# Kernel tuning notes

Hardware: AMD Instinct MI355X
Metric: run time of the kernel (lower is better)

## Reference

```python
import jax, jax.numpy as jnp
import numpy as np

N, C, H, W = 8, 128, 64, 64
S, K = 2, 5  # scale_factor, k_up
NK = (S * K) ** 2  # 100 predicted kernel channels
BN_EPS = 1e-5


def _conv(x, w, b, pad):
    y = jax.lax.conv_general_dilated(
        x, w, window_strides=(1, 1), padding=[(pad, pad), (pad, pad)],
        dimension_numbers=('NCHW', 'OIHW', 'NCHW'))
    return y + b[None, :, None, None]


def setup_inputs() -> dict:
    key = jax.random.key(0)
    ks = jax.random.split(key, 12)
    rn = lambda k, s, sc=0.05: jax.random.normal(k, s, jnp.float32) * sc
    return {
        'x': jax.random.normal(ks[0], (N, C, H, W), jnp.float32),
        'w_enc': rn(ks[1], (64, C, 3, 3)), 'b_enc': rn(ks[2], (64,)),
        'bn_gamma': jnp.ones((64,), jnp.float32), 'bn_beta': jnp.zeros((64,), jnp.float32),
        'bn_mean': rn(ks[3], (64,)), 'bn_var': jnp.abs(rn(ks[4], (64,))) + 1.0,
        'w_kp': rn(ks[5], (NK, 64, 1, 1)), 'b_kp': rn(ks[6], (NK,)),
        'w_g1': rn(ks[7], (64, 64, 3, 3)), 'b_g1': rn(ks[8], (64,)),
        'w_g2': rn(ks[9], (NK, 64, 1, 1)), 'b_g2': rn(ks[10], (NK,)),
    }


def reference(x, w_enc, b_enc, bn_gamma, bn_beta, bn_mean, bn_var,
              w_kp, b_kp, w_g1, b_g1, w_g2, b_g2):
    # content encoder: conv3x3 -> BN (inference stats) -> ReLU
    c = _conv(x, w_enc, b_enc, 1)
    inv = jax.lax.rsqrt(bn_var + BN_EPS)
    content = jax.nn.relu((c - bn_mean[None, :, None, None]) * (bn_gamma * inv)[None, :, None, None]
                          + bn_beta[None, :, None, None])
    # kernel and gate predictors
    kernel = _conv(content, w_kp, b_kp, 0)                     # (N, 100, H, W)
    gate = jax.nn.sigmoid(_conv(jax.nn.relu(_conv(content, w_g1, b_g1, 1)), w_g2, b_g2, 0))
    ker = jax.nn.softmax(kernel * gate, axis=1)                # softmax over all 100 chans
    ker = ker.reshape(N, K, K, S, S, H, W)
    # replicate-pad and gather KxK neighborhoods (channel-major, row-major kernel order = F.unfold)
    p = K // 2
    x_pad = jnp.pad(x, ((0, 0), (0, 0), (p, p), (p, p)), mode='edge')
    patches = jnp.stack([x_pad[:, :, i:i + H, j:j + W]
                         for i in range(K) for j in range(K)], axis=2)  # (N, C, K*K, H, W)
    patches = patches.reshape(N, C, K, K, H, W)
    # content-aware reassembly; target layout (N, C, H, S, W, S) for pixel-shuffle reshape
    out = jnp.einsum('ncijhw,nijsthw->nchswt', patches, ker)
    return out.reshape(N, C, H * S, W * S)
```

## Files before the change

### kernel.cpp

```cpp
#include <hip/hip_runtime.h>
#include <hip/hip_bf16.h>


typedef __attribute__((ext_vector_type(8))) short short8;
typedef __attribute__((ext_vector_type(4))) float f32x4;

__global__ __launch_bounds__(256) void x_to_bf_nhwc(const float* __restrict__ x,
                                                    __hip_bfloat16* __restrict__ xb) {
    __shared__ float ls[128 * 65];
    const int blk = blockIdx.x, n = blk >> 6, h = blk & 63;
    const int tid = threadIdx.x;
    for (int idx = tid; idx < 8192; idx += 256) {
        int ci = idx >> 6, w = idx & 63;
        ls[ci * 65 + w] = x[((n * 128 + ci) * 64 + h) * 64 + w];
    }
    __syncthreads();
    for (int idx = tid; idx < 8192; idx += 256) {
        int w = idx >> 7, ci = idx & 127;
        xb[((n * 64 + h) * 64 + w) * 128 + ci] = __float2bfloat16(ls[ci * 65 + w]);
    }
}

__global__ void w_to_bf(const float* __restrict__ w, __hip_bfloat16* __restrict__ o,
                        int CI, int total) {
    int idx = blockIdx.x * 256 + threadIdx.x;
    if (idx >= total) return;
    int ci = idx % CI;
    int t = idx / CI;
    int co = t & 63;
    int p = t >> 6;
    o[idx] = __float2bfloat16(w[(co * CI + ci) * 9 + p]);
}

template<int CIN>
__global__ __launch_bounds__(256) void conv3x3_mfma(
    const __hip_bfloat16* __restrict__ xb, const __hip_bfloat16* __restrict__ wt,
    const float* __restrict__ bias, const float* __restrict__ gamma,
    const float* __restrict__ beta, const float* __restrict__ mean,
    const float* __restrict__ var,
    float* __restrict__ out_f32,
    __hip_bfloat16* __restrict__ out_bf)
{
    constexpr int CINP = CIN + 8;
    __shared__ short xs[3 * 66 * CINP];
    const int blk = blockIdx.x, n = blk >> 6, h = blk & 63;
    const int tid = threadIdx.x;
    const int lane = tid & 63, wave = tid >> 6;
    const int m = lane & 15, q = lane >> 4;
    const int co0 = wave * 16;

    const short8 zero8 = {0, 0, 0, 0, 0, 0, 0, 0};
    for (int idx = tid; idx < 3 * 66 * (CIN / 8); idx += 256) {
        int c8 = idx % (CIN / 8);
        int p = idx / (CIN / 8);
        int r = p / 66, w = p % 66;
        int hh = h + r - 1, wc = w - 1;
        short8 v = zero8;
        if ((unsigned)hh < 64u && (unsigned)wc < 64u)
            v = *(const short8*)&xb[(((n * 64 + hh) * 64 + wc) * CIN) + c8 * 8];
        *(short8*)&xs[(r * 66 + w) * CINP + c8 * 8] = v;
    }
    __syncthreads();

    f32x4 acc[4] = {{0.f, 0.f, 0.f, 0.f}, {0.f, 0.f, 0.f, 0.f},
                    {0.f, 0.f, 0.f, 0.f}, {0.f, 0.f, 0.f, 0.f}};
    const int kbase = q * 8;
    #pragma unroll
    for (int kh = 0; kh < 3; ++kh) {
        #pragma unroll
        for (int kw = 0; kw < 3; ++kw) {
            const __hip_bfloat16* wp = &wt[((kh * 3 + kw) * 64 + co0 + m) * CIN + kbase];
            const short* xp = &xs[(kh * 66 + kw + m) * CINP + kbase];
            #pragma unroll
            for (int kc = 0; kc < CIN / 32; ++kc) {
                short8 bfrag = *(const short8*)&wp[kc * 32];
                #pragma unroll
                for (int mt = 0; mt < 4; ++mt) {
                    short8 afrag = *(const short8*)&xp[mt * 16 * CINP + kc * 32];
                    acc[mt] = __builtin_amdgcn_mfma_f32_16x16x32_bf16(
                        afrag, bfrag, acc[mt], 0, 0, 0);
                }
            }
        }
    }

    const int c = co0 + m;
    float sc, sh;
    if (gamma) {
        float inv = rsqrtf(var[c] + 1e-5f);
        sc = gamma[c] * inv;
        sh = (bias[c] - mean[c]) * sc + beta[c];
    } else {
        sc = 1.f;
        sh = bias[c];
    }
    #pragma unroll
    for (int mt = 0; mt < 4; ++mt) {
        const int w0 = mt * 16 + q * 4;
        float ov[4];
        #pragma unroll
        for (int r = 0; r < 4; ++r)
            ov[r] = fmaxf(fmaf(acc[mt][r], sc, sh), 0.f);
        if (out_f32) {
            #pragma unroll
            for (int r = 0; r < 4; ++r)
                out_f32[((n * 64 + h) * 64 + (w0 + r)) * 64 + c] = ov[r];
        }
        if (out_bf) {
            #pragma unroll
            for (int r = 0; r < 4; ++r)
                out_bf[((n * 64 + h) * 64 + (w0 + r)) * 64 + c] = __float2bfloat16(ov[r]);
        }
    }
}

__global__ __launch_bounds__(256) void predictor_k(
    const __hip_bfloat16* __restrict__ cb, const float* __restrict__ g1,
    const float* __restrict__ wkp, const float* __restrict__ bkp,
    const float* __restrict__ wg2, const float* __restrict__ bg2,
    float* __restrict__ ker)
{
    __shared__ float cs[64 * 68];
    __shared__ float gs[64 * 68];
    __shared__ float wsm[100 * 64];
    __shared__ float redm[256], reds[256];
    const int blk = blockIdx.x;
    const int n = blk >> 6, h = blk & 63;
    const int tid = threadIdx.x;
    const int w = tid & 63, qg = tid >> 6;

    for (int idx = tid; idx < 4096; idx += 256) {
        int ww = idx >> 6, ci = idx & 63;
        const int gidx = ((n * 64 + h) * 64 + ww) * 64 + ci;
        cs[ww * 68 + ci] = __bfloat162float(cb[gidx]);
        gs[ww * 68 + ci] = g1[gidx];
    }
    for (int idx = tid; idx < 6400; idx += 256) wsm[idx] = wkp[idx];
    __syncthreads();

    float ka[25], ga[25];
    #pragma unroll
    for (int j = 0; j < 25; ++j) ka[j] = bkp[qg * 25 + j];
    for (int ci = 0; ci < 64; ci += 4) {
        const float4 cv = *(const float4*)&cs[w * 68 + ci];
        #pragma unroll
        for (int j = 0; j < 25; ++j) {
            const float4 wv = *(const float4*)&wsm[(qg * 25 + j) * 64 + ci];
            ka[j] = fmaf(cv.x, wv.x, ka[j]);
            ka[j] = fmaf(cv.y, wv.y, ka[j]);
            ka[j] = fmaf(cv.z, wv.z, ka[j]);
            ka[j] = fmaf(cv.w, wv.w, ka[j]);
        }
    }
    __syncthreads();
    for (int idx = tid; idx < 6400; idx += 256) wsm[idx] = wg2[idx];
    __syncthreads();
    #pragma unroll
    for (int j = 0; j < 25; ++j) ga[j] = bg2[qg * 25 + j];
    for (int ci = 0; ci < 64; ci += 4) {
        const float4 gv = *(const float4*)&gs[w * 68 + ci];
        #pragma unroll
        for (int j = 0; j < 25; ++j) {
            const float4 wv = *(const float4*)&wsm[(qg * 25 + j) * 64 + ci];
            ga[j] = fmaf(gv.x, wv.x, ga[j]);
            ga[j] = fmaf(gv.y, wv.y, ga[j]);
            ga[j] = fmaf(gv.z, wv.z, ga[j]);
            ga[j] = fmaf(gv.w, wv.w, ga[j]);
        }
    }

    float p[25], m = -1e30f;
    #pragma unroll
    for (int j = 0; j < 25; ++j) {
        float s = 1.f / (1.f + __expf(-ga[j]));
        p[j] = ka[j] * s;
        m = fmaxf(m, p[j]);
    }
    redm[tid] = m;
    __syncthreads();
    m = fmaxf(fmaxf(redm[w], redm[64 + w]), fmaxf(redm[128 + w], redm[192 + w]));
    float ssum = 0.f;
    #pragma unroll
    for (int j = 0; j < 25; ++j) { p[j] = __expf(p[j] - m); ssum += p[j]; }
    reds[tid] = ssum;
    __syncthreads();
    ssum = reds[w] + reds[64 + w] + reds[128 + w] + reds[192 + w];
    const float r = 1.f / ssum;

    float* sm = cs;
    #pragma unroll
    for (int j = 0; j < 25; ++j) sm[w * 100 + qg * 25 + j] = p[j] * r;
    __syncthreads();
    const int base = (n * 64 + h) * 6400;
    for (int idx = tid; idx < 6400; idx += 256) ker[base + idx] = sm[idx];
}

__global__ __launch_bounds__(256) void reassembly_k(
    const float* __restrict__ x, const float* __restrict__ ker,
    float* __restrict__ out)
{
    constexpr int CT = 16;
    __shared__ float xls[CT][5][68];
    __shared__ float kls[64 * 108];
    const int blk = blockIdx.x;
    const int cb = blk & 7, h = (blk >> 3) & 63, n = blk >> 9;
    const int c0 = cb * CT;
    const int tid = threadIdx.x;
    const int w = tid & 63, cgq = tid >> 6;

    for (int idx = tid; idx < CT * 5 * 68; idx += 256) {
        int ci = idx / 340, r = idx % 340;
        int rr = r / 68, col = r % 68;
        int sr = min(max(h - 2 + rr, 0), 63);
        int sc = min(max(col - 2, 0), 63);
        xls[ci][rr][col] = x[((n * 128 + c0 + ci) * 64 + sr) * 64 + sc];
    }
    {
        const int base = (n * 64 + h) * 6400;
        for (int idx = tid; idx < 6400; idx += 256) {
            int ww = idx / 100, q = idx % 100;
            kls[ww * 108 + q] = ker[base + idx];
        }
    }
    __syncthreads();

    float acc[4][4] = {};
    #pragma unroll
    for (int i = 0; i < 5; ++i) {
        #pragma unroll
        for (int j = 0; j < 5; ++j) {
            const float4 kv = *(const float4*)&kls[w * 108 + (i * 5 + j) * 4];
            #pragma unroll
            for (int cc = 0; cc < 4; ++cc) {
                const float xv = xls[cgq * 4 + cc][i][w + j];
                acc[cc][0] = fmaf(xv, kv.x, acc[cc][0]);
                acc[cc][1] = fmaf(xv, kv.y, acc[cc][1]);
                acc[cc][2] = fmaf(xv, kv.z, acc[cc][2]);
                acc[cc][3] = fmaf(xv, kv.w, acc[cc][3]);
            }
        }
    }
    #pragma unroll
    for (int cc = 0; cc < 4; ++cc) {
        const int c = c0 + cgq * 4 + cc;
        #pragma unroll
        for (int s = 0; s < 2; ++s) {
            float2 v = make_float2(acc[cc][s * 2], acc[cc][s * 2 + 1]);
            *(float2*)&out[((n * 128 + c) * 128 + 2 * h + s) * 128 + 2 * w] = v;
        }
    }
}

extern "C" void kernel_launch(void* const* d_in, const int* in_sizes, int n_in,
                              void* d_out, int out_size, void* d_ws, size_t ws_size,
                              hipStream_t stream) {
    const float* x     = (const float*)d_in[0];
    const float* w_enc = (const float*)d_in[1];
    const float* b_enc = (const float*)d_in[2];
    const float* gamma = (const float*)d_in[3];
    const float* beta  = (const float*)d_in[4];
    const float* mean  = (const float*)d_in[5];
    const float* var   = (const float*)d_in[6];
    const float* w_kp  = (const float*)d_in[7];
    const float* b_kp  = (const float*)d_in[8];
    const float* w_g1  = (const float*)d_in[9];
    const float* b_g1  = (const float*)d_in[10];
    const float* w_g2  = (const float*)d_in[11];
    const float* b_g2  = (const float*)d_in[12];
    float* out = (float*)d_out;

    float* g1r = (float*)d_ws;
    float* ker = g1r + 2097152;
    __hip_bfloat16* xb  = (__hip_bfloat16*)(ker + 3276800);
    __hip_bfloat16* cbf = xb + 4194304;
    __hip_bfloat16* wtt = cbf + 2097152;
    __hip_bfloat16* wgt = wtt + 73728;

    x_to_bf_nhwc<<<512, 256, 0, stream>>>(x, xb);
    w_to_bf<<<288, 256, 0, stream>>>(w_enc, wtt, 128, 73728);
    w_to_bf<<<144, 256, 0, stream>>>(w_g1, wgt, 64, 36864);

    conv3x3_mfma<128><<<512, 256, 0, stream>>>(
        xb, wtt, b_enc, gamma, beta, mean, var, nullptr, cbf);
    conv3x3_mfma<64><<<512, 256, 0, stream>>>(
        cbf, wgt, b_g1, nullptr, nullptr, nullptr, nullptr, g1r, nullptr);

    predictor_k<<<512, 256, 0, stream>>>(cbf, g1r, w_kp, b_kp, w_g2, b_g2, ker);
    reassembly_k<<<4096, 256, 0, stream>>>(x, ker, out);
}
```

Baseline: 217.1 us.

## Split conv rows into half-width blocks and stream reassembly kernels from global

The 3x3 MFMA convs now process half a row per block, with waves tiled 2x2 over width and output channels, doubling the grid to 1024 blocks and shrinking shared memory. Reassembly loads x rows with float4 vector loads plus explicit edge replication, and reads the per-pixel kernel weights straight from global memory instead of staging them in LDS. This targets occupancy, shared-memory footprint and load efficiency, at the cost of more halo reloads in the conv and uncached strided global reads of ker in reassembly. The CINP padding also changes from 8 to 4, which affects LDS bank conflicts and short8 alignment.

```diff
diff --git a/kernel.cpp b/kernel.cpp
--- a/kernel.cpp
+++ b/kernel.cpp
@@ -41,75 +41,67 @@
     float* __restrict__ out_f32,
     __hip_bfloat16* __restrict__ out_bf)
 {
-    constexpr int CINP = CIN + 8;
-    __shared__ short xs[3 * 66 * CINP];
-    const int blk = blockIdx.x, n = blk >> 6, h = blk & 63;
+    constexpr int CINP = CIN + 4;
+    __shared__ short xs[3 * 34 * CINP];
+    const int blk = blockIdx.x;
+    const int wh = blk & 1, h = (blk >> 1) & 63, n = blk >> 7;
     const int tid = threadIdx.x;
     const int lane = tid & 63, wave = tid >> 6;
     const int m = lane & 15, q = lane >> 4;
-    const int co0 = wave * 16;
+    const int mt = wave >> 1;
+    const int nh = wave & 1;
 
     const short8 zero8 = {0, 0, 0, 0, 0, 0, 0, 0};
-    for (int idx = tid; idx < 3 * 66 * (CIN / 8); idx += 256) {
+    for (int idx = tid; idx < 3 * 34 * (CIN / 8); idx += 256) {
         int c8 = idx % (CIN / 8);
         int p = idx / (CIN / 8);
-        int r = p / 66, w = p % 66;
-        int hh = h + r - 1, wc = w - 1;
+        int r = p / 34, cx = p % 34;
+        int hh = h + r - 1, gc = wh * 32 - 1 + cx;
         short8 v = zero8;
-        if ((unsigned)hh < 64u && (unsigned)wc < 64u)
-            v = *(const short8*)&xb[(((n * 64 + hh) * 64 + wc) * CIN) + c8 * 8];
-        *(short8*)&xs[(r * 66 + w) * CINP + c8 * 8] = v;
-    }
-    __syncthreads();
-
-    f32x4 acc[4] = {{0.f, 0.f, 0.f, 0.f}, {0.f, 0.f, 0.f, 0.f},
-                    {0.f, 0.f, 0.f, 0.f}, {0.f, 0.f, 0.f, 0.f}};
+        if ((unsigned)hh < 64u && (unsigned)gc < 64u)
+            v = *(const short8*)&xb[(((n * 64 + hh) * 64 + gc) * CIN) + c8 * 8];
+        *(short8*)&xs[(r * 34 + cx) * CINP + c8 * 8] = v;
+    }
+    __syncthreads();
+
+    f32x4 acc[2] = {{0.f, 0.f, 0.f, 0.f}, {0.f, 0.f, 0.f, 0.f}};
     const int kbase = q * 8;
     #pragma unroll
     for (int kh = 0; kh < 3; ++kh) {
         #pragma unroll
         for (int kw = 0; kw < 3; ++kw) {
-            const __hip_bfloat16* wp = &wt[((kh * 3 + kw) * 64 + co0 + m) * CIN + kbase];
-            const short* xp = &xs[(kh * 66 + kw + m) * CINP + kbase];
+            const short* xp = &xs[(kh * 34 + mt * 16 + m + kw) * CINP + kbase];
+            const __hip_bfloat16* wp = &wt[((kh * 3 + kw) * 64 + nh * 32 + m) * CIN + kbase];
             #pragma unroll
             for (int kc = 0; kc < CIN / 32; ++kc) {
-                short8 bfrag = *(const short8*)&wp[kc * 32];
-                #pragma unroll
-                for (int mt = 0; mt < 4; ++mt) {
-                    short8 afrag = *(const short8*)&xp[mt * 16 * CINP + kc * 32];
-                    acc[mt] = __builtin_amdgcn_mfma_f32_16x16x32_bf16(
-                        afrag, bfrag, acc[mt], 0, 0, 0);
-                }
+                short8 afrag = *(const short8*)&xp[kc * 32];
+                short8 b0 = *(const short8*)&wp[kc * 32];
+                short8 b1 = *(const short8*)&wp[16 * CIN + kc * 32];
+                acc[0] = __builtin_amdgcn_mfma_f32_16x16x32_bf16(afrag, b0, acc[0], 0, 0, 0);
+                acc[1] = __builtin_amdgcn_mfma_f32_16x16x32_bf16(afrag, b1, acc[1], 0, 0, 0);
             }
         }
     }
 
-    const int c = co0 + m;
-    float sc, sh;
-    if (gamma) {
-        float inv = rsqrtf(var[c] + 1e-5f);
-        sc = gamma[c] * inv;
-        sh = (bias[c] - mean[c]) * sc + beta[c];
-    } else {
-        sc = 1.f;
-        sh = bias[c];
-    }
-    #pragma unroll
-    for (int mt = 0; mt < 4; ++mt) {
-        const int w0 = mt * 16 + q * 4;
-        float ov[4];
-        #pragma unroll
-        for (int r = 0; r < 4; ++r)
-            ov[r] = fmaxf(fmaf(acc[mt][r], sc, sh), 0.f);
-        if (out_f32) {
-            #pragma unroll
-            for (int r = 0; r < 4; ++r)
-                out_f32[((n * 64 + h) * 64 + (w0 + r)) * 64 + c] = ov[r];
-        }
-        if (out_bf) {
-            #pragma unroll
-            for (int r = 0; r < 4; ++r)
-                out_bf[((n * 64 + h) * 64 + (w0 + r)) * 64 + c] = __float2bfloat16(ov[r]);
+    #pragma unroll
+    for (int nt = 0; nt < 2; ++nt) {
+        const int c = nh * 32 + nt * 16 + m;
+        float sc, sh;
+        if (gamma) {
+            float inv = rsqrtf(var[c] + 1e-5f);
+            sc = gamma[c] * inv;
+            sh = (bias[c] - mean[c]) * sc + beta[c];
+        } else {
+            sc = 1.f;
+            sh = bias[c];
+        }
+        const int w0 = wh * 32 + mt * 16 + q * 4;
+        #pragma unroll
+        for (int r = 0; r < 4; ++r) {
+            float ov = fmaxf(fmaf(acc[nt][r], sc, sh), 0.f);
+            const int gi = ((n * 64 + h) * 64 + (w0 + r)) * 64 + c;
+            if (out_f32) out_f32[gi] = ov;
+            if (out_bf)  out_bf[gi] = __float2bfloat16(ov);
         }
     }
 }
@@ -201,38 +193,40 @@
 {
     constexpr int CT = 16;
     __shared__ float xls[CT][5][68];
-    __shared__ float kls[64 * 108];
     const int blk = blockIdx.x;
     const int cb = blk & 7, h = (blk >> 3) & 63, n = blk >> 9;
     const int c0 = cb * CT;
     const int tid = threadIdx.x;
-    const int w = tid & 63, cgq = tid >> 6;
-
-    for (int idx = tid; idx < CT * 5 * 68; idx += 256) {
-        int ci = idx / 340, r = idx % 340;
-        int rr = r / 68, col = r % 68;
+    const int w = tid & 63, cg = tid >> 6;
+
+    for (int idx = tid; idx < CT * 5 * 16; idx += 256) {
+        int c = idx / 80, r2 = idx % 80;
+        int rr = r2 / 16, c4 = r2 % 16;
         int sr = min(max(h - 2 + rr, 0), 63);
-        int sc = min(max(col - 2, 0), 63);
-        xls[ci][rr][col] = x[((n * 128 + c0 + ci) * 64 + sr) * 64 + sc];
-    }
-    {
-        const int base = (n * 64 + h) * 6400;
-        for (int idx = tid; idx < 6400; idx += 256) {
-            int ww = idx / 100, q = idx % 100;
-            kls[ww * 108 + q] = ker[base + idx];
-        }
-    }
-    __syncthreads();
-
+        float4 v = *(const float4*)&x[((n * 128 + c0 + c) * 64 + sr) * 64 + c4 * 4];
+        *(float2*)&xls[c][rr][2 + c4 * 4] = make_float2(v.x, v.y);
+        *(float2*)&xls[c][rr][4 + c4 * 4] = make_float2(v.z, v.w);
+    }
+    if (tid < CT * 5) {
+        int c = tid / 5, rr = tid % 5;
+        int sr = min(max(h - 2 + rr, 0), 63);
+        float xl = x[((n * 128 + c0 + c) * 64 + sr) * 64 + 0];
+        float xr = x[((n * 128 + c0 + c) * 64 + sr) * 64 + 63];
+        xls[c][rr][0] = xl; xls[c][rr][1] = xl;
+        xls[c][rr][66] = xr; xls[c][rr][67] = xr;
+    }
+    __syncthreads();
+
+    const float* kp = &ker[((n * 64 + h) * 64 + w) * 100];
     float acc[4][4] = {};
     #pragma unroll
     for (int i = 0; i < 5; ++i) {
         #pragma unroll
         for (int j = 0; j < 5; ++j) {
-            const float4 kv = *(const float4*)&kls[w * 108 + (i * 5 + j) * 4];
+            const float4 kv = *(const float4*)&kp[(i * 5 + j) * 4];
             #pragma unroll
             for (int cc = 0; cc < 4; ++cc) {
-                const float xv = xls[cgq * 4 + cc][i][w + j];
+                const float xv = xls[cg * 4 + cc][i][w + j];
                 acc[cc][0] = fmaf(xv, kv.x, acc[cc][0]);
                 acc[cc][1] = fmaf(xv, kv.y, acc[cc][1]);
                 acc[cc][2] = fmaf(xv, kv.z, acc[cc][2]);
@@ -242,7 +236,7 @@
     }
     #pragma unroll
     for (int cc = 0; cc < 4; ++cc) {
-        const int c = c0 + cgq * 4 + cc;
+        const int c = c0 + cg * 4 + cc;
         #pragma unroll
         for (int s = 0; s < 2; ++s) {
             float2 v = make_float2(acc[cc][s * 2], acc[cc][s * 2 + 1]);
@@ -280,9 +274,9 @@
     w_to_bf<<<288, 256, 0, stream>>>(w_enc, wtt, 128, 73728);
     w_to_bf<<<144, 256, 0, stream>>>(w_g1, wgt, 64, 36864);
 
-    conv3x3_mfma<128><<<512, 256, 0, stream>>>(
+    conv3x3_mfma<128><<<1024, 256, 0, stream>>>(
         xb, wtt, b_enc, gamma, beta, mean, var, nullptr, cbf);
-    conv3x3_mfma<64><<<512, 256, 0, stream>>>(
+    conv3x3_mfma<64><<<1024, 256, 0, stream>>>(
         cbf, wgt, b_g1, nullptr, nullptr, nullptr, nullptr, g1r, nullptr);
 
     predictor_k<<<512, 256, 0, stream>>>(cbf, g1r, w_kp, b_kp, w_g2, b_g2, ker);
```

After: 236.1 us. 8.7% more time.
